# Kernel optimization log

Hardware: AMD Instinct MI355X
Metric: run time of the kernel (lower is better)

Reference implementation:

```python
import jax, jax.numpy as jnp
import numpy as np

EMB_SIZE = 1024  # scale uses model dim per original code (not head_size)

def setup_inputs() -> dict:
    key = jax.random.key(0)
    k1, k2, k3, k4 = jax.random.split(key, 4)
    B, T, E, H = 4, 4096, 1024, 64
    x = jax.random.normal(k1, (B, T, E), dtype=jnp.float32)
    Wq = jax.random.normal(k2, (E, H), dtype=jnp.float32) * (E ** -0.5)
    Wk = jax.random.normal(k3, (E, H), dtype=jnp.float32) * (E ** -0.5)
    Wv = jax.random.normal(k4, (E, H), dtype=jnp.float32) * (E ** -0.5)
    return {"x": x, "Wq": Wq, "Wk": Wk, "Wv": Wv}

def reference(x, Wq, Wk, Wv):
    B, T, E = x.shape
    q = x @ Wq  # [B,T,H]
    k = x @ Wk
    v = x @ Wv
    scale = E ** -0.5  # original scales by emb_size, not head_size
    scores = jnp.einsum('bth,bsh->bts', q, k) * scale  # [B,T,T]
    causal = jnp.tril(jnp.ones((T, T), dtype=bool))
    scores = jnp.where(causal, scores, -jnp.inf)
    weights = jax.nn.softmax(scores, axis=-1)
    # dropout is identity in eval mode (deterministic baseline)
    return jnp.einsum('bts,bsh->bth', weights, v)
```

## Files before the change

### kernel.cpp

```cpp
#include <hip/hip_runtime.h>
#include <hip/hip_bf16.h>

typedef __bf16 bf16_t;
typedef __bf16 bf16x4 __attribute__((ext_vector_type(4)));
typedef __bf16 bf16x8 __attribute__((ext_vector_type(8)));
typedef float f32x4 __attribute__((ext_vector_type(4)));

#define MFMA16(a, b, c) __builtin_amdgcn_mfma_f32_16x16x32_bf16(a, b, c, 0, 0, 0)

static constexpr float LOG2E = 1.44269504088896340736f;
static constexpr float QSCALE = LOG2E / 32.0f;


__device__ __forceinline__ void gload_lds16(const bf16_t* src, bf16_t* dst) {
    __builtin_amdgcn_global_load_lds(
        (const __attribute__((address_space(1))) void*)src,
        (__attribute__((address_space(3))) void*)dst, 16, 0, 0);
}

template <int CTRL>
__device__ __forceinline__ float dppf(float v) {
    return __builtin_bit_cast(
        float, __builtin_amdgcn_mov_dpp(__builtin_bit_cast(int, v), CTRL, 0xf, 0xf, true));
}
__device__ __forceinline__ float rmax16(float t) {
    t = fmaxf(t, dppf<0xB1>(t));
    t = fmaxf(t, dppf<0x4E>(t));
    t = fmaxf(t, dppf<0x141>(t));
    t = fmaxf(t, dppf<0x140>(t));
    return t;
}
__device__ __forceinline__ float rsum16(float t) {
    t += dppf<0xB1>(t);
    t += dppf<0x4E>(t);
    t += dppf<0x141>(t);
    t += dppf<0x140>(t);
    return t;
}

__global__ __launch_bounds__(256) void transpose_w_kernel(const float* __restrict__ Wq,
                                                          const float* __restrict__ Wk,
                                                          const float* __restrict__ Wv,
                                                          bf16_t* __restrict__ wt) {
    __shared__ float tile[64][68];
    int w = blockIdx.x >> 4;
    int e0 = (blockIdx.x & 15) * 64;
    const float* W = (w == 0) ? Wq : ((w == 1) ? Wk : Wv);
    int t = threadIdx.x;
    int r = t >> 2, q = t & 3;
    const float* src = W + (size_t)(e0 + r) * 64 + q * 16;
#pragma unroll
    for (int jj = 0; jj < 4; ++jj) {
        float4 v = *(const float4*)(src + jj * 4);
        *(float4*)&tile[r][q * 16 + jj * 4] = v;
    }
    __syncthreads();
    bf16_t* dst = wt + (size_t)w * 65536 + (size_t)r * 1024 + e0 + q * 16;
    bf16x8 o0, o1;
#pragma unroll
    for (int jj = 0; jj < 8; ++jj) o0[jj] = (bf16_t)tile[q * 16 + jj][r];
#pragma unroll
    for (int jj = 0; jj < 8; ++jj) o1[jj] = (bf16_t)tile[q * 16 + 8 + jj][r];
    *(bf16x8*)dst = o0;
    *(bf16x8*)(dst + 8) = o1;
}

__global__ __launch_bounds__(256) void proj_kernel(const float* __restrict__ x,
                                                   const bf16_t* __restrict__ wt,
                                                   bf16_t* __restrict__ qs,
                                                   bf16_t* __restrict__ ks,
                                                   bf16_t* __restrict__ vt) {
    __shared__ __align__(16) bf16_t xa[2][32 * 128];
    __shared__ __align__(16) bf16_t wb[2][96 * 128];
    __shared__ float vred[64][33];

    int tid = threadIdx.x;
    int wave = tid >> 6, lane = tid & 63;
    int lr = lane & 15, lg = lane >> 4;
    int wr = wave >> 1, wc = wave & 1;
    int bid = blockIdx.x;
    int h2 = bid & 1;
    int r0 = (bid >> 1) << 5;

    const bf16_t* wtb = wt + (size_t)h2 * 96 * 1024;

    int xrow0 = tid >> 4, xe0 = tid & 15;
    int xrow1 = (tid + 256) >> 4, xe1 = tid & 15;
    const float* xs0 = x + (size_t)(r0 + xrow0) * 1024 + ((xe0 ^ (xrow0 & 15)) * 8);
    const float* xs1 = x + (size_t)(r0 + xrow1) * 1024 + ((xe1 ^ (xrow1 & 15)) * 8);
    int wubase = tid & ~63;

    f32x4 a0 = {0.f, 0.f, 0.f, 0.f}, a1 = a0, a2 = a0;

#pragma unroll
    for (int call = 0; call < 6; ++call) {
        int u = call * 256 + tid;
        int col = u >> 4, ep = u & 15;
        gload_lds16(wtb + (size_t)col * 1024 + ((ep ^ (col & 15)) * 8),
                    &wb[0][(size_t)(call * 256 + wubase) * 8]);
    }
    {
        float4 p00 = *(const float4*)(xs0);
        float4 p01 = *(const float4*)(xs0 + 4);
        float4 p10 = *(const float4*)(xs1);
        float4 p11 = *(const float4*)(xs1 + 4);
        bf16x8 w0, w1;
        w0[0] = (bf16_t)p00.x; w0[1] = (bf16_t)p00.y; w0[2] = (bf16_t)p00.z; w0[3] = (bf16_t)p00.w;
        w0[4] = (bf16_t)p01.x; w0[5] = (bf16_t)p01.y; w0[6] = (bf16_t)p01.z; w0[7] = (bf16_t)p01.w;
        w1[0] = (bf16_t)p10.x; w1[1] = (bf16_t)p10.y; w1[2] = (bf16_t)p10.z; w1[3] = (bf16_t)p10.w;
        w1[4] = (bf16_t)p11.x; w1[5] = (bf16_t)p11.y; w1[6] = (bf16_t)p11.z; w1[7] = (bf16_t)p11.w;
        *(bf16x8*)&xa[0][(size_t)tid * 8] = w0;
        *(bf16x8*)&xa[0][(size_t)(tid + 256) * 8] = w1;
    }
    __syncthreads();

    for (int c = 0; c < 8; ++c) {
        int cur = c & 1;
        float4 p00, p01, p10, p11;
        if (c < 7) {
            int k0 = (c + 1) * 128;
#pragma unroll
            for (int call = 0; call < 6; ++call) {
                int u = call * 256 + tid;
                int col = u >> 4, ep = u & 15;
                gload_lds16(wtb + (size_t)col * 1024 + k0 + ((ep ^ (col & 15)) * 8),
                            &wb[cur ^ 1][(size_t)(call * 256 + wubase) * 8]);
            }
            p00 = *(const float4*)(xs0 + k0);
            p01 = *(const float4*)(xs0 + k0 + 4);
            p10 = *(const float4*)(xs1 + k0);
            p11 = *(const float4*)(xs1 + k0 + 4);
        }

#pragma unroll
        for (int sub = 0; sub < 4; ++sub) {
            int eu = sub * 4 + lg;
            bf16x8 af = *(const bf16x8*)&xa[cur][(size_t)((wr * 16 + lr) * 16 + (eu ^ lr)) * 8];
            bf16x8 b0 = *(const bf16x8*)&wb[cur][(size_t)((wc * 48 + lr) * 16 + (eu ^ lr)) * 8];
            bf16x8 b1 = *(const bf16x8*)&wb[cur][(size_t)((wc * 48 + 16 + lr) * 16 + (eu ^ lr)) * 8];
            bf16x8 b2 = *(const bf16x8*)&wb[cur][(size_t)((wc * 48 + 32 + lr) * 16 + (eu ^ lr)) * 8];
            a0 = MFMA16(af, b0, a0);
            a1 = MFMA16(af, b1, a1);
            a2 = MFMA16(af, b2, a2);
        }

        if (c < 7) {
            bf16x8 w0, w1;
            w0[0] = (bf16_t)p00.x; w0[1] = (bf16_t)p00.y; w0[2] = (bf16_t)p00.z; w0[3] = (bf16_t)p00.w;
            w0[4] = (bf16_t)p01.x; w0[5] = (bf16_t)p01.y; w0[6] = (bf16_t)p01.z; w0[7] = (bf16_t)p01.w;
            w1[0] = (bf16_t)p10.x; w1[1] = (bf16_t)p10.y; w1[2] = (bf16_t)p10.z; w1[3] = (bf16_t)p10.w;
            w1[4] = (bf16_t)p11.x; w1[5] = (bf16_t)p11.y; w1[6] = (bf16_t)p11.z; w1[7] = (bf16_t)p11.w;
            *(bf16x8*)&xa[cur ^ 1][(size_t)tid * 8] = w0;
            *(bf16x8*)&xa[cur ^ 1][(size_t)(tid + 256) * 8] = w1;
        }
        __syncthreads();
    }

    f32x4 accs[3] = {a0, a1, a2};
#pragma unroll
    for (int cc = 0; cc < 3; ++cc) {
        int gcol = h2 * 96 + wc * 48 + cc * 16 + lr;
        int w3 = gcol >> 6, h = gcol & 63;
#pragma unroll
        for (int r = 0; r < 4; ++r) {
            int lrow = wr * 16 + lg * 4 + r;
            int row = r0 + lrow;
            float v = accs[cc][r];
            if (w3 == 0) {
                qs[(size_t)row * 64 + h] = (bf16_t)(v * QSCALE);
            } else if (w3 == 1) {
                ks[(size_t)row * 64 + h] = (bf16_t)v;
            } else {
                vred[h][lrow] = v;
            }
        }
    }
    if (h2 == 1) {
        __syncthreads();
        int h = tid >> 2, j8 = (tid & 3) * 8;
        int bb = r0 >> 12, t0 = r0 & 4095;
        bf16x8 v8;
#pragma unroll
        for (int jj = 0; jj < 8; ++jj) v8[jj] = (bf16_t)vred[h][j8 + jj];
        *(bf16x8*)(vt + ((size_t)(bb * 64 + h)) * 4096 + t0 + j8) = v8;
    }
}

__global__ __launch_bounds__(256) void attn_kernel(const bf16_t* __restrict__ qs,
                                                   const bf16_t* __restrict__ ks,
                                                   const bf16_t* __restrict__ vt,
                                                   bf16_t* __restrict__ po,
                                                   float* __restrict__ pm,
                                                   float* __restrict__ pls) {
    __shared__ __align__(16) bf16_t kt[2][64 * 64];
    __shared__ __align__(16) bf16_t vtl[2][64 * 64];
    __shared__ __align__(16) bf16_t pl[4][16][80];

    int tid = threadIdx.x;
    int wave = tid >> 6, lane = tid & 63;
    int lr = lane & 15, lg = lane >> 4;

    int bid = blockIdx.x;
    int s = bid & 3;
    int jq = (bid >> 2) & 63;
    int b = bid >> 8;
    int qt = (jq & 1) ? (63 - (jq >> 1)) : (jq >> 1);
    int q0 = qt << 6;
    int nk = qt + 1;
    int lo = (nk * s) >> 2;
    int hi = (nk * (s + 1)) >> 2;
    int ntile = hi - lo;

    int srow = tid >> 3, sc = tid & 7;
    int sw8 = srow & 7;
    int koff0 = srow * 64 + ((sc ^ sw8) * 8);
    int koff1 = (32 + srow) * 64 + ((sc ^ sw8) * 8);
    const bf16_t* kg = ks + ((size_t)b * 4096) * 64;
    const bf16_t* vg = vt + ((size_t)b * 64) * 4096;

    const bf16_t* qb = qs + (size_t)(b * 4096 + q0 + wave * 16 + lr) * 64 + lg * 8;
    bf16x8 qf0 = *(const bf16x8*)qb;
    bf16x8 qf1 = *(const bf16x8*)(qb + 32);

    f32x4 o[4];
    float m[4], l[4];
#pragma unroll
    for (int r = 0; r < 4; ++r) {
        o[r] = (f32x4){0.f, 0.f, 0.f, 0.f};
        m[r] = -INFINITY;
        l[r] = 0.f;
    }

    bf16x8 kr0, kr1, vr0, vr1;
    if (ntile > 0) {
        int kb = lo << 6;
        kr0 = *(const bf16x8*)(kg + (size_t)(kb + srow) * 64 + sc * 8);
        kr1 = *(const bf16x8*)(kg + (size_t)(kb + 32 + srow) * 64 + sc * 8);
        vr0 = *(const bf16x8*)(vg + (size_t)srow * 4096 + kb + sc * 8);
        vr1 = *(const bf16x8*)(vg + (size_t)(32 + srow) * 4096 + kb + sc * 8);
    }

    for (int ti = 0; ti < ntile; ++ti) {
        int cur = ti & 1;
        *(bf16x8*)(&kt[cur][koff0]) = kr0;
        *(bf16x8*)(&kt[cur][koff1]) = kr1;
        *(bf16x8*)(&vtl[cur][koff0]) = vr0;
        *(bf16x8*)(&vtl[cur][koff1]) = vr1;
        __syncthreads();
        if (ti + 1 < ntile) {
            int kb = (lo + ti + 1) << 6;
            kr0 = *(const bf16x8*)(kg + (size_t)(kb + srow) * 64 + sc * 8);
            kr1 = *(const bf16x8*)(kg + (size_t)(kb + 32 + srow) * 64 + sc * 8);
            vr0 = *(const bf16x8*)(vg + (size_t)srow * 4096 + kb + sc * 8);
            vr1 = *(const bf16x8*)(vg + (size_t)(32 + srow) * 4096 + kb + sc * 8);
        }

        int gt = lo + ti;
        int kb = gt << 6;
        const bf16_t* kbuf = kt[cur];
        const bf16_t* vbuf = vtl[cur];

        f32x4 z = {0.f, 0.f, 0.f, 0.f};
        f32x4 sv[4];
#pragma unroll
        for (int g = 0; g < 4; ++g) {
            int krow = g * 16 + lr;
            int sw = krow & 7;
            bf16x8 kf0 = *(const bf16x8*)(kbuf + krow * 64 + ((lg ^ sw) * 8));
            bf16x8 kf1 = *(const bf16x8*)(kbuf + krow * 64 + (((4 | lg) ^ sw) * 8));
            sv[g] = MFMA16(qf0, kf0, z);
            sv[g] = MFMA16(qf1, kf1, sv[g]);
        }

        if (gt == nk - 1) {
#pragma unroll
            for (int r = 0; r < 4; ++r) {
                int qrow = q0 + wave * 16 + lg * 4 + r;
#pragma unroll
                for (int g = 0; g < 4; ++g)
                    if (kb + g * 16 + lr > qrow) sv[g][r] = -INFINITY;
            }
        }

#pragma unroll
        for (int r = 0; r < 4; ++r) {
            float t2 = fmaxf(fmaxf(sv[0][r], sv[1][r]), fmaxf(sv[2][r], sv[3][r]));
            t2 = rmax16(t2);
            float mn = fmaxf(m[r], t2);
            float a = __builtin_amdgcn_exp2f(m[r] - mn);
            float p0 = __builtin_amdgcn_exp2f(sv[0][r] - mn);
            float p1 = __builtin_amdgcn_exp2f(sv[1][r] - mn);
            float p2 = __builtin_amdgcn_exp2f(sv[2][r] - mn);
            float p3 = __builtin_amdgcn_exp2f(sv[3][r] - mn);
            float rs = rsum16((p0 + p1) + (p2 + p3));
            l[r] = l[r] * a + rs;
            m[r] = mn;
            o[0][r] *= a; o[1][r] *= a; o[2][r] *= a; o[3][r] *= a;
            int prow = lg * 4 + r;
            pl[wave][prow][lr] = (bf16_t)p0;
            pl[wave][prow][16 + lr] = (bf16_t)p1;
            pl[wave][prow][32 + lr] = (bf16_t)p2;
            pl[wave][prow][48 + lr] = (bf16_t)p3;
        }

        bf16x8 pa0 = *(const bf16x8*)&pl[wave][lr][lg * 8];
        bf16x8 pa1 = *(const bf16x8*)&pl[wave][lr][32 + lg * 8];
#pragma unroll
        for (int oc = 0; oc < 4; ++oc) {
            int drow = oc * 16 + lr;
            int sw = drow & 7;
            bf16x8 vf0 = *(const bf16x8*)(vbuf + drow * 64 + ((lg ^ sw) * 8));
            bf16x8 vf1 = *(const bf16x8*)(vbuf + drow * 64 + (((4 | lg) ^ sw) * 8));
            o[oc] = MFMA16(pa0, vf0, o[oc]);
            o[oc] = MFMA16(pa1, vf1, o[oc]);
        }
    }

    size_t pblk = ((size_t)((b << 6) + qt) << 2) + s;
    bf16_t* pop = po + pblk * 4096;
#pragma unroll
    for (int r = 0; r < 4; ++r) {
        int row = wave * 16 + lg * 4 + r;
#pragma unroll
        for (int oc = 0; oc < 4; ++oc) pop[row * 64 + oc * 16 + lr] = (bf16_t)o[oc][r];
        if (lr == r) {
            pm[pblk * 64 + row] = m[r];
            pls[pblk * 64 + row] = l[r];
        }
    }
}

__global__ __launch_bounds__(256) void merge_kernel(const bf16_t* __restrict__ po,
                                                    const float* __restrict__ pm,
                                                    const float* __restrict__ pls,
                                                    float* __restrict__ out) {
    int gid = blockIdx.x * 256 + threadIdx.x;
    int row = gid >> 2, cq = gid & 3;
    int b = row >> 12, t = row & 4095;
    int qt = t >> 6, lrow = t & 63;
    int pb = ((b << 6) + qt) << 2;

    float mm[4], w[4];
    float M = -INFINITY;
#pragma unroll
    for (int i = 0; i < 4; ++i) {
        mm[i] = pm[(size_t)(pb + i) * 64 + lrow];
        M = fmaxf(M, mm[i]);
    }
    float L = 0.f;
#pragma unroll
    for (int i = 0; i < 4; ++i) {
        w[i] = (mm[i] == -INFINITY) ? 0.f : __builtin_amdgcn_exp2f(mm[i] - M);
        L += pls[(size_t)(pb + i) * 64 + lrow] * w[i];
    }
    float rL = 1.0f / L;

    float acc[16];
#pragma unroll
    for (int j = 0; j < 16; ++j) acc[j] = 0.f;
#pragma unroll
    for (int i = 0; i < 4; ++i) {
        const bf16_t* p = po + ((size_t)(pb + i) * 64 + lrow) * 64 + cq * 16;
        bf16x8 x0 = *(const bf16x8*)p, x1 = *(const bf16x8*)(p + 8);
#pragma unroll
        for (int j = 0; j < 8; ++j) acc[j] += w[i] * (float)x0[j];
#pragma unroll
        for (int j = 0; j < 8; ++j) acc[8 + j] += w[i] * (float)x1[j];
    }
    float* op = out + (size_t)row * 64 + cq * 16;
#pragma unroll
    for (int j = 0; j < 16; ++j) op[j] = acc[j] * rL;
}

extern "C" void kernel_launch(void* const* d_in, const int* in_sizes, int n_in,
                              void* d_out, int out_size, void* d_ws, size_t ws_size,
                              hipStream_t stream) {
    const float* x  = (const float*)d_in[0];
    const float* Wq = (const float*)d_in[1];
    const float* Wk = (const float*)d_in[2];
    const float* Wv = (const float*)d_in[3];
    float* out = (float*)d_out;

    char* ws = (char*)d_ws;
    bf16_t* qs = (bf16_t*)(ws);
    bf16_t* ks = (bf16_t*)(ws + (2u << 20));
    bf16_t* vt = (bf16_t*)(ws + (4u << 20));
    bf16_t* wt = (bf16_t*)(ws + (6u << 20));
    bf16_t* po = (bf16_t*)(ws + (8u << 20));
    float*  pm = (float*)(ws + (16u << 20));
    float*  pls = (float*)(ws + (16u << 20) + (256u << 10));

    transpose_w_kernel<<<48, 256, 0, stream>>>(Wq, Wk, Wv, wt);
    proj_kernel<<<1024, 256, 0, stream>>>(x, wt, qs, ks, vt);
    attn_kernel<<<1024, 256, 0, stream>>>(qs, ks, vt, po, pm, pls);
    merge_kernel<<<256, 256, 0, stream>>>(po, pm, pls, out);
}
```

Before: 174.4 us.

## Halve projection K-chunk with deeper x prefetch, add lazy softmax rescaling

The projection kernel now works in 64-wide K chunks with smaller LDS buffers and a two-chunk-ahead register prefetch of x, which is meant to cut LDS use and raise occupancy. The V transpose staging buffer is now bf16, so the final store is one vector read instead of eight scalar conversions. In attention, the running max and the rescaling of l and o only update when some row's max grows by more than 8 (log2 units), so the exp2 and multiply work is skipped on most tiles. The cost is a warp-wide vote per tile, and unnormalised probabilities can reach up to 2^8 before bf16 rounding.

```diff
diff --git a/kernel.cpp b/kernel.cpp
--- a/kernel.cpp
+++ b/kernel.cpp
@@ -70,9 +70,9 @@
                                                    bf16_t* __restrict__ qs,
                                                    bf16_t* __restrict__ ks,
                                                    bf16_t* __restrict__ vt) {
-    __shared__ __align__(16) bf16_t xa[2][32 * 128];
-    __shared__ __align__(16) bf16_t wb[2][96 * 128];
-    __shared__ float vred[64][33];
+    __shared__ __align__(16) bf16_t xa[2][32 * 64];
+    __shared__ __align__(16) bf16_t wb[2][96 * 64];
+    __shared__ __align__(16) bf16_t vredb[64][40];
 
     int tid = threadIdx.x;
     int wave = tid >> 6, lane = tid & 63;
@@ -83,80 +83,75 @@
     int r0 = (bid >> 1) << 5;
 
     const bf16_t* wtb = wt + (size_t)h2 * 96 * 1024;
-
-    int xrow0 = tid >> 4, xe0 = tid & 15;
-    int xrow1 = (tid + 256) >> 4, xe1 = tid & 15;
-    const float* xs0 = x + (size_t)(r0 + xrow0) * 1024 + ((xe0 ^ (xrow0 & 15)) * 8);
-    const float* xs1 = x + (size_t)(r0 + xrow1) * 1024 + ((xe1 ^ (xrow1 & 15)) * 8);
     int wubase = tid & ~63;
 
-    f32x4 a0 = {0.f, 0.f, 0.f, 0.f}, a1 = a0, a2 = a0;
-
-#pragma unroll
-    for (int call = 0; call < 6; ++call) {
+    int xrow = tid >> 3, xep = tid & 7;
+    const float* xsrc = x + (size_t)(r0 + xrow) * 1024 + xep * 8;
+    bf16_t* xdst0 = &xa[0][(size_t)(xrow * 8 + (xep ^ (xrow & 7))) * 8];
+    bf16_t* xdst1 = &xa[1][(size_t)(xrow * 8 + (xep ^ (xrow & 7))) * 8];
+
+    f32x4 acc[3];
+#pragma unroll
+    for (int cc = 0; cc < 3; ++cc) acc[cc] = (f32x4){0.f, 0.f, 0.f, 0.f};
+
+#pragma unroll
+    for (int call = 0; call < 3; ++call) {
         int u = call * 256 + tid;
-        int col = u >> 4, ep = u & 15;
-        gload_lds16(wtb + (size_t)col * 1024 + ((ep ^ (col & 15)) * 8),
+        int col = u >> 3, ep = u & 7;
+        gload_lds16(wtb + (size_t)col * 1024 + ((ep ^ (col & 7)) * 8),
                     &wb[0][(size_t)(call * 256 + wubase) * 8]);
     }
     {
-        float4 p00 = *(const float4*)(xs0);
-        float4 p01 = *(const float4*)(xs0 + 4);
-        float4 p10 = *(const float4*)(xs1);
-        float4 p11 = *(const float4*)(xs1 + 4);
-        bf16x8 w0, w1;
-        w0[0] = (bf16_t)p00.x; w0[1] = (bf16_t)p00.y; w0[2] = (bf16_t)p00.z; w0[3] = (bf16_t)p00.w;
-        w0[4] = (bf16_t)p01.x; w0[5] = (bf16_t)p01.y; w0[6] = (bf16_t)p01.z; w0[7] = (bf16_t)p01.w;
-        w1[0] = (bf16_t)p10.x; w1[1] = (bf16_t)p10.y; w1[2] = (bf16_t)p10.z; w1[3] = (bf16_t)p10.w;
-        w1[4] = (bf16_t)p11.x; w1[5] = (bf16_t)p11.y; w1[6] = (bf16_t)p11.z; w1[7] = (bf16_t)p11.w;
-        *(bf16x8*)&xa[0][(size_t)tid * 8] = w0;
-        *(bf16x8*)&xa[0][(size_t)(tid + 256) * 8] = w1;
-    }
+        float4 ca = *(const float4*)(xsrc);
+        float4 cb = *(const float4*)(xsrc + 4);
+        bf16x8 w0;
+        w0[0] = (bf16_t)ca.x; w0[1] = (bf16_t)ca.y; w0[2] = (bf16_t)ca.z; w0[3] = (bf16_t)ca.w;
+        w0[4] = (bf16_t)cb.x; w0[5] = (bf16_t)cb.y; w0[6] = (bf16_t)cb.z; w0[7] = (bf16_t)cb.w;
+        *(bf16x8*)xdst0 = w0;
+    }
+    float4 fa0 = *(const float4*)(xsrc + 64), fa1 = *(const float4*)(xsrc + 68);
+    float4 fb0 = *(const float4*)(xsrc + 128), fb1 = *(const float4*)(xsrc + 132);
     __syncthreads();
 
-    for (int c = 0; c < 8; ++c) {
+    for (int c = 0; c < 16; ++c) {
         int cur = c & 1;
-        float4 p00, p01, p10, p11;
-        if (c < 7) {
-            int k0 = (c + 1) * 128;
-#pragma unroll
-            for (int call = 0; call < 6; ++call) {
+        if (c < 15) {
+            int k0 = (c + 1) * 64;
+#pragma unroll
+            for (int call = 0; call < 3; ++call) {
                 int u = call * 256 + tid;
-                int col = u >> 4, ep = u & 15;
-                gload_lds16(wtb + (size_t)col * 1024 + k0 + ((ep ^ (col & 15)) * 8),
+                int col = u >> 3, ep = u & 7;
+                gload_lds16(wtb + (size_t)col * 1024 + k0 + ((ep ^ (col & 7)) * 8),
                             &wb[cur ^ 1][(size_t)(call * 256 + wubase) * 8]);
             }
-            p00 = *(const float4*)(xs0 + k0);
-            p01 = *(const float4*)(xs0 + k0 + 4);
-            p10 = *(const float4*)(xs1 + k0);
-            p11 = *(const float4*)(xs1 + k0 + 4);
-        }
-
-#pragma unroll
-        for (int sub = 0; sub < 4; ++sub) {
-            int eu = sub * 4 + lg;
-            bf16x8 af = *(const bf16x8*)&xa[cur][(size_t)((wr * 16 + lr) * 16 + (eu ^ lr)) * 8];
-            bf16x8 b0 = *(const bf16x8*)&wb[cur][(size_t)((wc * 48 + lr) * 16 + (eu ^ lr)) * 8];
-            bf16x8 b1 = *(const bf16x8*)&wb[cur][(size_t)((wc * 48 + 16 + lr) * 16 + (eu ^ lr)) * 8];
-            bf16x8 b2 = *(const bf16x8*)&wb[cur][(size_t)((wc * 48 + 32 + lr) * 16 + (eu ^ lr)) * 8];
-            a0 = MFMA16(af, b0, a0);
-            a1 = MFMA16(af, b1, a1);
-            a2 = MFMA16(af, b2, a2);
-        }
-
-        if (c < 7) {
-            bf16x8 w0, w1;
-            w0[0] = (bf16_t)p00.x; w0[1] = (bf16_t)p00.y; w0[2] = (bf16_t)p00.z; w0[3] = (bf16_t)p00.w;
-            w0[4] = (bf16_t)p01.x; w0[5] = (bf16_t)p01.y; w0[6] = (bf16_t)p01.z; w0[7] = (bf16_t)p01.w;
-            w1[0] = (bf16_t)p10.x; w1[1] = (bf16_t)p10.y; w1[2] = (bf16_t)p10.z; w1[3] = (bf16_t)p10.w;
-            w1[4] = (bf16_t)p11.x; w1[5] = (bf16_t)p11.y; w1[6] = (bf16_t)p11.z; w1[7] = (bf16_t)p11.w;
-            *(bf16x8*)&xa[cur ^ 1][(size_t)tid * 8] = w0;
-            *(bf16x8*)&xa[cur ^ 1][(size_t)(tid + 256) * 8] = w1;
+        }
+
+        int arow = wr * 16 + lr;
+#pragma unroll
+        for (int ksi = 0; ksi < 2; ++ksi) {
+            bf16x8 af = *(const bf16x8*)&xa[cur][(size_t)(arow * 8 + ((ksi * 4 + lg) ^ (arow & 7))) * 8];
+#pragma unroll
+            for (int cc = 0; cc < 3; ++cc) {
+                int bcol = wc * 48 + cc * 16 + lr;
+                bf16x8 bf = *(const bf16x8*)&wb[cur][(size_t)(bcol * 8 + ((ksi * 4 + lg) ^ (bcol & 7))) * 8];
+                acc[cc] = MFMA16(af, bf, acc[cc]);
+            }
+        }
+
+        if (c < 15) {
+            bf16x8 w0;
+            w0[0] = (bf16_t)fa0.x; w0[1] = (bf16_t)fa0.y; w0[2] = (bf16_t)fa0.z; w0[3] = (bf16_t)fa0.w;
+            w0[4] = (bf16_t)fa1.x; w0[5] = (bf16_t)fa1.y; w0[6] = (bf16_t)fa1.z; w0[7] = (bf16_t)fa1.w;
+            *(bf16x8*)((cur ^ 1) ? xdst1 : xdst0) = w0;
+            fa0 = fb0; fa1 = fb1;
+            if (c + 3 < 16) {
+                fb0 = *(const float4*)(xsrc + (c + 3) * 64);
+                fb1 = *(const float4*)(xsrc + (c + 3) * 64 + 4);
+            }
         }
         __syncthreads();
     }
 
-    f32x4 accs[3] = {a0, a1, a2};
 #pragma unroll
     for (int cc = 0; cc < 3; ++cc) {
         int gcol = h2 * 96 + wc * 48 + cc * 16 + lr;
@@ -165,13 +160,13 @@
         for (int r = 0; r < 4; ++r) {
             int lrow = wr * 16 + lg * 4 + r;
             int row = r0 + lrow;
-            float v = accs[cc][r];
+            float v = acc[cc][r];
             if (w3 == 0) {
                 qs[(size_t)row * 64 + h] = (bf16_t)(v * QSCALE);
             } else if (w3 == 1) {
                 ks[(size_t)row * 64 + h] = (bf16_t)v;
             } else {
-                vred[h][lrow] = v;
+                vredb[gcol & 63][lrow] = (bf16_t)v;
             }
         }
     }
@@ -179,9 +174,7 @@
         __syncthreads();
         int h = tid >> 2, j8 = (tid & 3) * 8;
         int bb = r0 >> 12, t0 = r0 & 4095;
-        bf16x8 v8;
-#pragma unroll
-        for (int jj = 0; jj < 8; ++jj) v8[jj] = (bf16_t)vred[h][j8 + jj];
+        bf16x8 v8 = *(const bf16x8*)&vredb[h][j8];
         *(bf16x8*)(vt + ((size_t)(bb * 64 + h)) * 4096 + t0 + j8) = v8;
     }
 }
@@ -282,20 +275,32 @@
             }
         }
 
+        float t2v[4];
 #pragma unroll
         for (int r = 0; r < 4; ++r) {
             float t2 = fmaxf(fmaxf(sv[0][r], sv[1][r]), fmaxf(sv[2][r], sv[3][r]));
-            t2 = rmax16(t2);
-            float mn = fmaxf(m[r], t2);
-            float a = __builtin_amdgcn_exp2f(m[r] - mn);
-            float p0 = __builtin_amdgcn_exp2f(sv[0][r] - mn);
-            float p1 = __builtin_amdgcn_exp2f(sv[1][r] - mn);
-            float p2 = __builtin_amdgcn_exp2f(sv[2][r] - mn);
-            float p3 = __builtin_amdgcn_exp2f(sv[3][r] - mn);
+            t2v[r] = rmax16(t2);
+        }
+        float grow = fmaxf(fmaxf(t2v[0] - m[0], t2v[1] - m[1]),
+                           fmaxf(t2v[2] - m[2], t2v[3] - m[3]));
+        if (!__all(grow <= 8.0f)) {
+#pragma unroll
+            for (int r = 0; r < 4; ++r) {
+                float mn = fmaxf(m[r], t2v[r]);
+                float a = __builtin_amdgcn_exp2f(m[r] - mn);
+                l[r] *= a;
+                o[0][r] *= a; o[1][r] *= a; o[2][r] *= a; o[3][r] *= a;
+                m[r] = mn;
+            }
+        }
+#pragma unroll
+        for (int r = 0; r < 4; ++r) {
+            float p0 = __builtin_amdgcn_exp2f(sv[0][r] - m[r]);
+            float p1 = __builtin_amdgcn_exp2f(sv[1][r] - m[r]);
+            float p2 = __builtin_amdgcn_exp2f(sv[2][r] - m[r]);
+            float p3 = __builtin_amdgcn_exp2f(sv[3][r] - m[r]);
             float rs = rsum16((p0 + p1) + (p2 + p3));
-            l[r] = l[r] * a + rs;
-            m[r] = mn;
-            o[0][r] *= a; o[1][r] *= a; o[2][r] *= a; o[3][r] *= a;
+            l[r] += rs;
             int prow = lg * 4 + r;
             pl[wave][prow][lr] = (bf16_t)p0;
             pl[wave][prow][16 + lr] = (bf16_t)p1;
```

New measurement: 163.8 us. -6.1%, faster.
